# Kernel optimization log

Hardware: AMD Instinct MI355X
Metric: run time of the kernel (lower is better)

## Reference

```python
import jax, jax.numpy as jnp
import numpy as np

KH = KW = 3
STRIDE = 1
PAD = 1
DIL = 1


def im2col(x, kh, kw, stride, pad, dil):
    """F.unfold equivalent: x (N,C,H,W) -> (N,C,kh,kw,oh,ow)."""
    n, c, h, w = x.shape
    oh = (h + 2 * pad - dil * (kh - 1) - 1) // stride + 1
    ow = (w + 2 * pad - dil * (kw - 1) - 1) // stride + 1
    xp = jnp.pad(x, ((0, 0), (0, 0), (pad, pad), (pad, pad)))
    rows = []
    for i in range(kh):
        cols = []
        for j in range(kw):
            patch = jax.lax.slice(
                xp,
                (0, 0, i * dil, j * dil),
                (n, c, i * dil + (oh - 1) * stride + 1, j * dil + (ow - 1) * stride + 1),
                (1, 1, stride, stride),
            )  # (N,C,oh,ow)
            cols.append(patch)
        rows.append(jnp.stack(cols, axis=2))  # (N,C,kw,oh,ow)
    return jnp.stack(rows, axis=2)  # (N,C,kh,kw,oh,ow)


def setup_inputs() -> dict:
    key = jax.random.key(0)
    k1, k2, k3, k4 = jax.random.split(key, 4)
    N, Cin, Cout, H, W = 4, 64, 64, 128, 128
    x = jax.random.normal(k1, (N, Cin, H, W), dtype=jnp.float32)
    # adapting kernel: positive values (softmax-like output in EdgeKernel2d)
    kernel = jax.random.uniform(k2, (N, 1, KH, KW, H, W), dtype=jnp.float32, minval=0.01, maxval=1.0)
    fan_in = Cin * KH * KW
    weight = jax.random.normal(k3, (Cout, Cin, KH, KW), dtype=jnp.float32) * (1.0 / np.sqrt(fan_in))
    bias = jax.random.normal(k4, (Cout,), dtype=jnp.float32) * 0.01
    return {"x": x, "kernel": kernel, "weight": weight, "bias": bias}


def reference(x, kernel, weight, bias):
    # im_cols: (N,Cin,kh,kw,oh,ow)
    im_cols = im2col(x, KH, KW, STRIDE, PAD, DIL)
    in_mul_k = im_cols * kernel  # kernel broadcasts over Cin
    # dominate = sum_{k,l} in_mul_k / sum_{k,l} kernel  -> (N,Cin,oh,ow)
    dominate = in_mul_k.sum(axis=(2, 3)) / kernel.sum(axis=(2, 3))
    corrected = in_mul_k + dominate[:, :, None, None] * (1.0 - kernel)
    out = jnp.einsum('ncklhw,ockl->nohw', corrected, weight)
    out = out + bias[None, :, None, None]
    return out
```

## Files before the change

kernel.cpp:

```cpp
#include <hip/hip_runtime.h>
#include <hip/hip_bf16.h>
#include <cstddef>

typedef __attribute__((ext_vector_type(8))) short bf16x8;
typedef __attribute__((ext_vector_type(4))) float f32x4;
typedef __attribute__((ext_vector_type(2))) unsigned int u32x2;

#define NB 4
#define CIN 64
#define COUT 64
#define HH 128
#define WW 128
#define TAPS 9
#define KCH 160
#define KTOT 640
#define STRD 82

__device__ __forceinline__ unsigned short f2bf(float f) {
    union { float f; unsigned u; } v; v.f = f;
    unsigned u = v.u + 0x7FFFu + ((v.u >> 16) & 1u);
    return (unsigned short)(u >> 16);
}

__global__ void prep_weight(const float* __restrict__ w, unsigned short* __restrict__ wB,
                            float* __restrict__ zrow) {
    int idx = blockIdx.x * blockDim.x + threadIdx.x;
    if (idx < 192) zrow[idx] = 0.f;
    if (idx >= COUT * KTOT) return;
    int o = idx / KTOT;
    int kk = idx - o * KTOT;
    int chunk = kk / KCH;
    int kl = kk - chunk * KCH;
    unsigned short v = 0;
    if (kl < 16 * TAPS) {
        int tap = kl >> 4;
        int cl = kl & 15;
        v = f2bf(w[(o * CIN + chunk * 16 + cl) * TAPS + tap]);
    }
    wB[idx] = v;
}

__launch_bounds__(256)
__global__ void pac_conv(const float* __restrict__ x, const float* __restrict__ Kp,
                         const unsigned short* __restrict__ wB,
                         const float* __restrict__ bias,
                         const float* __restrict__ zrow1,
                         float* __restrict__ out) {
    __shared__ unsigned int sCor[64][STRD];

    const int blk0 = blockIdx.x;
    const int blk  = ((blk0 & 7) << 7) | (blk0 >> 3);

    const int w0 = (blk & 1) * 64;
    const int h  = (blk >> 1) & (HH - 1);
    const int n  = blk >> 8;
    const int t    = threadIdx.x;
    const int lane = t & 63;
    const int wv   = __builtin_amdgcn_readfirstlane(t >> 6);

    float kreg[TAPS];
    float ks = 0.f;
    const float* kp = Kp + ((size_t)n * TAPS * HH + h) * WW + w0 + lane;
    #pragma unroll
    for (int tap = 0; tap < TAPS; ++tap) {
        kreg[tap] = kp[(size_t)tap * HH * WW];
        ks += kreg[tap];
    }
    const float inv = 1.0f / ks;

    for (int i = t; i < 64 * 8; i += 256) sCor[i >> 3][72 + (i & 7)] = 0u;

    const bool mL = (w0 == 0) && (lane == 0);
    const bool mR = (w0 != 0) && (lane == 63);
    const unsigned voffL = (mL ? 1u : (unsigned)lane) * 4u;
    const unsigned voffC = ((unsigned)lane + 1u) * 4u;
    const unsigned voffR = (mR ? 64u : (unsigned)lane + 2u) * 4u;

    const int l15 = lane & 15;
    const int g   = lane >> 4;
    const float bval = bias[wv * 16 + l15];

    f32x4 acc[4];
    #pragma unroll
    for (int i = 0; i < 4; ++i) acc[i] = (f32x4){0.f, 0.f, 0.f, 0.f};

    for (int chunk = 0; chunk < 4; ++chunk) {
        const int c0 = chunk * 16 + wv * 4;
        const float* xb = x + (size_t)(n * CIN + c0) * (HH * WW) + w0 - 1;

        float xv[4][TAPS];
        #pragma unroll
        for (int j = 0; j < 4; ++j) {
            #pragma unroll
            for (int k = 0; k < 3; ++k) {
                const int hh2 = h + k - 1;
                const float* p = ((unsigned)hh2 < (unsigned)HH)
                    ? (xb + (size_t)j * (HH * WW) + (size_t)hh2 * WW)
                    : (zrow1 - 1);
                float vL = *(const float*)((const char*)p + voffL);
                float vC = *(const float*)((const char*)p + voffC);
                float vR = *(const float*)((const char*)p + voffR);
                xv[j][k * 3 + 0] = mL ? 0.f : vL;
                xv[j][k * 3 + 1] = vC;
                xv[j][k * 3 + 2] = mR ? 0.f : vR;
            }
        }

        float dom[4];
        #pragma unroll
        for (int j = 0; j < 4; ++j) {
            float s = 0.f;
            #pragma unroll
            for (int tap = 0; tap < TAPS; ++tap) s = fmaf(xv[j][tap], kreg[tap], s);
            dom[j] = s * inv;
        }
        u32x2 cor[TAPS];
        #pragma unroll
        for (int tap = 0; tap < TAPS; ++tap) {
            float c0f = fmaf(kreg[tap], xv[0][tap] - dom[0], dom[0]);
            float c1f = fmaf(kreg[tap], xv[1][tap] - dom[1], dom[1]);
            float c2f = fmaf(kreg[tap], xv[2][tap] - dom[2], dom[2]);
            float c3f = fmaf(kreg[tap], xv[3][tap] - dom[3], dom[3]);
            union { __hip_bfloat162 h2; unsigned int u; } a, b;
            a.h2 = __float22bfloat162_rn(make_float2(c0f, c1f));
            b.h2 = __float22bfloat162_rn(make_float2(c2f, c3f));
            cor[tap] = (u32x2){a.u, b.u};
        }

        if (chunk) __syncthreads();
        #pragma unroll
        for (int tap = 0; tap < TAPS; ++tap)
            *reinterpret_cast<u32x2*>(&sCor[lane][tap * 8 + wv * 2]) = cor[tap];
        __syncthreads();

        const unsigned short* wrow = wB + (size_t)(wv * 16 + l15) * KTOT + chunk * KCH + g * 8;
        #pragma unroll
        for (int step = 0; step < 5; ++step) {
            bf16x8 bfrag = *reinterpret_cast<const bf16x8*>(wrow + step * 32);
            #pragma unroll
            for (int pt = 0; pt < 4; ++pt) {
                const unsigned int* ap = &sCor[pt * 16 + l15][step * 16 + g * 4];
                u32x2 alo = *reinterpret_cast<const u32x2*>(ap);
                u32x2 ahi = *reinterpret_cast<const u32x2*>(ap + 2);
                union { u32x2 p[2]; bf16x8 f; } af;
                af.p[0] = alo; af.p[1] = ahi;
                acc[pt] = __builtin_amdgcn_mfma_f32_16x16x32_bf16(af.f, bfrag, acc[pt], 0, 0, 0);
            }
        }
    }

    const int o = wv * 16 + l15;
    float* op = out + (((size_t)n * COUT + o) * HH + h) * WW + w0 + g * 4;
    #pragma unroll
    for (int pt = 0; pt < 4; ++pt) {
        f32x4 v = acc[pt];
        #pragma unroll
        for (int r = 0; r < 4; ++r) v[r] += bval;
        *reinterpret_cast<f32x4*>(op + pt * 16) = v;
    }
}

extern "C" void kernel_launch(void* const* d_in, const int* in_sizes, int n_in,
                              void* d_out, int out_size, void* d_ws, size_t ws_size,
                              hipStream_t stream) {
    const float* x    = (const float*)d_in[0];
    const float* Kp   = (const float*)d_in[1];
    const float* wgt  = (const float*)d_in[2];
    const float* bias = (const float*)d_in[3];
    float* out = (float*)d_out;
    unsigned short* wB = (unsigned short*)d_ws;
    float* zrow = (float*)((char*)d_ws + 81920);

    prep_weight<<<(COUT * KTOT + 255) / 256, 256, 0, stream>>>(wgt, wB, zrow);

    pac_conv<<<NB * HH * (WW / 64), 256, 0, stream>>>(x, Kp, wB, bias, zrow + 1, out);
}
```

Measured before the change: 29.03 us.

## Share neighbor columns via DPP wave shifts and prefetch weight fragments

```diff
diff --git a/kernel.cpp b/kernel.cpp
--- a/kernel.cpp
+++ b/kernel.cpp
@@ -15,6 +15,15 @@
 #define KCH 160
 #define KTOT 640
 #define STRD 82
+
+__device__ __forceinline__ float dpp_shr1(float v) {
+    int r = __builtin_amdgcn_update_dpp(0, __builtin_bit_cast(int, v), 0x138, 0xF, 0xF, true);
+    return __builtin_bit_cast(float, r);
+}
+__device__ __forceinline__ float dpp_shl1(float v) {
+    int r = __builtin_amdgcn_update_dpp(0, __builtin_bit_cast(int, v), 0x130, 0xF, 0xF, true);
+    return __builtin_bit_cast(float, r);
+}
 
 __device__ __forceinline__ unsigned short f2bf(float f) {
     union { float f; unsigned u; } v; v.f = f;
@@ -44,7 +53,7 @@
 __global__ void pac_conv(const float* __restrict__ x, const float* __restrict__ Kp,
                          const unsigned short* __restrict__ wB,
                          const float* __restrict__ bias,
-                         const float* __restrict__ zrow1,
+                         const float* __restrict__ zrowp,
                          float* __restrict__ out) {
     __shared__ unsigned int sCor[64][STRD];
 
@@ -70,11 +79,8 @@
 
     for (int i = t; i < 64 * 8; i += 256) sCor[i >> 3][72 + (i & 7)] = 0u;
 
-    const bool mL = (w0 == 0) && (lane == 0);
-    const bool mR = (w0 != 0) && (lane == 63);
-    const unsigned voffL = (mL ? 1u : (unsigned)lane) * 4u;
-    const unsigned voffC = ((unsigned)lane + 1u) * 4u;
-    const unsigned voffR = (mR ? 64u : (unsigned)lane + 2u) * 4u;
+    const int  hlane = (w0 == 0) ? 63 : 0;
+    const int  hofs  = (w0 == 0) ? 64 : -1;
 
     const int l15 = lane & 15;
     const int g   = lane >> 4;
@@ -84,28 +90,48 @@
     #pragma unroll
     for (int i = 0; i < 4; ++i) acc[i] = (f32x4){0.f, 0.f, 0.f, 0.f};
 
-    for (int chunk = 0; chunk < 4; ++chunk) {
-        const int c0 = chunk * 16 + wv * 4;
-        const float* xb = x + (size_t)(n * CIN + c0) * (HH * WW) + w0 - 1;
-
-        float xv[4][TAPS];
+    #pragma unroll
+    for (int it = 0; it < 4; ++it) {
+        const int cr = (it + blk) & 3;
+        const int c0 = cr * 16 + wv * 4;
+        const float* xb0 = x + (size_t)(n * CIN + c0) * (HH * WW);
+
+        const unsigned short* wrow = wB + (size_t)(wv * 16 + l15) * KTOT + cr * KCH + g * 8;
+        bf16x8 bu[5];
+        #pragma unroll
+        for (int s = 0; s < 5; ++s) bu[s] = *reinterpret_cast<const bf16x8*>(wrow + s * 32);
+
+        float vc[4][3], hv[4][3];
         #pragma unroll
         for (int j = 0; j < 4; ++j) {
             #pragma unroll
             for (int k = 0; k < 3; ++k) {
                 const int hh2 = h + k - 1;
-                const float* p = ((unsigned)hh2 < (unsigned)HH)
-                    ? (xb + (size_t)j * (HH * WW) + (size_t)hh2 * WW)
-                    : (zrow1 - 1);
-                float vL = *(const float*)((const char*)p + voffL);
-                float vC = *(const float*)((const char*)p + voffC);
-                float vR = *(const float*)((const char*)p + voffR);
-                xv[j][k * 3 + 0] = mL ? 0.f : vL;
+                const float* rp = ((unsigned)hh2 < (unsigned)HH)
+                    ? (xb0 + (size_t)j * (HH * WW) + (size_t)hh2 * WW + w0)
+                    : zrowp;
+                vc[j][k] = rp[lane];
+                float hvv = 0.f;
+                if (lane == hlane) hvv = rp[hofs];
+                hv[j][k] = hvv;
+            }
+        }
+
+        float xv[4][TAPS];
+        #pragma unroll
+        for (int j = 0; j < 4; ++j) {
+            #pragma unroll
+            for (int k = 0; k < 3; ++k) {
+                const float vC = vc[j][k];
+                float vL = dpp_shr1(vC);
+                float vR = dpp_shl1(vC);
+                if (w0 == 0) { if (lane == 63) vR = hv[j][k]; }
+                else         { if (lane == 0)  vL = hv[j][k]; }
+                xv[j][k * 3 + 0] = vL;
                 xv[j][k * 3 + 1] = vC;
-                xv[j][k * 3 + 2] = mR ? 0.f : vR;
+                xv[j][k * 3 + 2] = vR;
             }
         }
-
         float dom[4];
         #pragma unroll
         for (int j = 0; j < 4; ++j) {
@@ -127,16 +153,14 @@
             cor[tap] = (u32x2){a.u, b.u};
         }
 
-        if (chunk) __syncthreads();
+        if (it) __syncthreads();
         #pragma unroll
         for (int tap = 0; tap < TAPS; ++tap)
             *reinterpret_cast<u32x2*>(&sCor[lane][tap * 8 + wv * 2]) = cor[tap];
         __syncthreads();
 
-        const unsigned short* wrow = wB + (size_t)(wv * 16 + l15) * KTOT + chunk * KCH + g * 8;
         #pragma unroll
         for (int step = 0; step < 5; ++step) {
-            bf16x8 bfrag = *reinterpret_cast<const bf16x8*>(wrow + step * 32);
             #pragma unroll
             for (int pt = 0; pt < 4; ++pt) {
                 const unsigned int* ap = &sCor[pt * 16 + l15][step * 16 + g * 4];
@@ -144,7 +168,7 @@
                 u32x2 ahi = *reinterpret_cast<const u32x2*>(ap + 2);
                 union { u32x2 p[2]; bf16x8 f; } af;
                 af.p[0] = alo; af.p[1] = ahi;
-                acc[pt] = __builtin_amdgcn_mfma_f32_16x16x32_bf16(af.f, bfrag, acc[pt], 0, 0, 0);
+                acc[pt] = __builtin_amdgcn_mfma_f32_16x16x32_bf16(af.f, bu[step], acc[pt], 0, 0, 0);
             }
         }
     }
```

Result: slower. 30.57 us (+5.3%).
